# Optimization experiments

Hardware: AMD Instinct MI355X
Metric: run time of the kernel (lower is better)

The kernel has to match this reference:

```python
import jax, jax.numpy as jnp
import numpy as np

N = 50000      # num nodes
E = 800000     # num edges
F_IN = 100     # input features (ogbn-products)
HID = 128      # hidden_dim (per-head out_channels)
H = 2          # heads
OUT = 47       # num classes
NEG_SLOPE = 0.2


def setup_inputs() -> dict:
    key = jax.random.key(0)
    ks = jax.random.split(key, 14)
    def glorot(k, shape, fan):
        return jax.random.normal(k, shape, jnp.float32) * (1.0 / np.sqrt(fan))
    x = jax.random.normal(ks[0], (N, F_IN), jnp.float32)
    edge_index = jax.random.randint(ks[1], (2, E), 0, N)
    # GAT layer 0: lin_l (= lin_r, shared) weight [H*HID, F_IN], attention vecs [H, HID]
    W0 = glorot(ks[2], (H * HID, F_IN), F_IN)
    b0 = jnp.zeros((H * HID,), jnp.float32)
    attl0 = glorot(ks[3], (H, HID), HID)
    attr0 = glorot(ks[4], (H, HID), HID)
    # GAT layer 1: input dim H*HID
    W1 = glorot(ks[5], (H * HID, H * HID), H * HID)
    b1 = jnp.zeros((H * HID,), jnp.float32)
    attl1 = glorot(ks[6], (H, HID), HID)
    attr1 = glorot(ks[7], (H, HID), HID)
    # post_mp: Linear(H*HID -> HID), Linear(HID -> OUT)
    Wp1 = glorot(ks[8], (HID, H * HID), H * HID)
    bp1 = jnp.zeros((HID,), jnp.float32)
    Wp2 = glorot(ks[9], (OUT, HID), HID)
    bp2 = jnp.zeros((OUT,), jnp.float32)
    return dict(x=x, edge_index=edge_index, W0=W0, b0=b0, attl0=attl0, attr0=attr0,
                W1=W1, b1=b1, attl1=attl1, attr1=attr1,
                Wp1=Wp1, bp1=bp1, Wp2=Wp2, bp2=bp2)


def gat_layer(x, W, b, att_l, att_r, src, dst):
    # shared lin_l == lin_r in the source
    h = (x @ W.T + b).reshape(-1, H, HID)          # [N, H, C]
    alpha_l = jnp.einsum('nhc,hc->nh', h, att_l)   # per-node left scores
    alpha_r = jnp.einsum('nhc,hc->nh', h, att_r)   # per-node right scores
    e = jax.nn.leaky_relu(alpha_l[src] + alpha_r[dst], NEG_SLOPE)  # [E, H]
    # segment softmax over edges grouped by destination node
    emax = jax.ops.segment_max(e, dst, num_segments=N)             # [N, H]
    ee = jnp.exp(e - emax[dst])
    denom = jax.ops.segment_sum(ee, dst, num_segments=N)           # [N, H]
    a = ee / denom[dst]                                            # [E, H]
    msg = a[:, :, None] * h[src]                                   # [E, H, C]
    out = jax.ops.segment_sum(msg, dst, num_segments=N)            # [N, H, C]
    return out.reshape(-1, H * HID)


def reference(x, edge_index, W0, b0, attl0, attr0, W1, b1, attl1, attr1, Wp1, bp1, Wp2, bp2):
    src, dst = edge_index[0], edge_index[1]
    x = jax.nn.relu(gat_layer(x, W0, b0, attl0, attr0, src, dst))
    x = jax.nn.relu(gat_layer(x, W1, b1, attl1, attr1, src, dst))
    h = x @ Wp1.T + bp1           # dropout p=0.0 -> identity
    logits = h @ Wp2.T + bp2
    return jax.nn.log_softmax(logits, axis=1)
```

## Files before the change

### kernel.cpp

```cpp
#include <hip/hip_runtime.h>
#include <math.h>

#define N_NODES 50000
#define E_EDGES 800000
#define F_IN 100
#define HID 128
#define HEADS 2
#define OUT_C 47
#define HH (HEADS*HID)
#define MPAD 50176
#define SLOTS 64

typedef float floatx4 __attribute__((ext_vector_type(4)));
typedef float float2v __attribute__((ext_vector_type(2)));
typedef short short8 __attribute__((ext_vector_type(8)));

__device__ inline ushort bf16round(float v) {
    unsigned u = __float_as_uint(v);
    return (ushort)((u + 0x7FFFu + ((u >> 16) & 1u)) >> 16);
}

__device__ __forceinline__ void gl_lds16(const void* g, void* l) {
    __builtin_amdgcn_global_load_lds(
        (const __attribute__((address_space(1))) unsigned int*)g,
        (__attribute__((address_space(3))) unsigned int*)l, 16, 0, 0);
}

__device__ __forceinline__ void gemm_body(
    int bx, int by,
    const ushort* __restrict__ Ab, const ushort* __restrict__ Wb,
    const float* __restrict__ bias,
    ushort* __restrict__ Hb,
    const float* __restrict__ attl, const float* __restrict__ attr,
    float* __restrict__ al, float* __restrict__ ar,
    int M, int Kp, ushort* sA, ushort* sB)
{
    const int t = threadIdx.x;
    const int wave = t >> 6, lane = t & 63;
    const int quad = lane >> 4, l16 = lane & 15;
    const int rl = lane >> 2, seg = lane & 3;
    const int m0 = by * 64, n0 = bx * 128;

    floatx4 acc[8];
#pragma unroll
    for (int j = 0; j < 8; j++) acc[j] = (floatx4)(0.f);

    for (int k0 = 0; k0 < Kp; k0 += 32) {
        {
            size_t gro = (size_t)(m0 + wave * 16 + rl) * Kp + k0 + seg * 8;
            gl_lds16(Ab + gro, sA + (wave * 16) * 32);
        }
#pragma unroll
        for (int j = 0; j < 2; j++) {
            int br = wave * 32 + j * 16;
            size_t gro = (size_t)(n0 + br + rl) * Kp + k0 + seg * 8;
            gl_lds16(Wb + gro, sB + br * 32);
        }
        __syncthreads();

        short8 af = *(const short8*)(sA + (wave * 16 + l16) * 32 + quad * 8);
#pragma unroll
        for (int sn = 0; sn < 8; sn++) {
            int r = sn * 16 + l16;
            short8 b = *(const short8*)(sB + r * 32 + quad * 8);
            acc[sn] = __builtin_amdgcn_mfma_f32_16x16x32_bf16(af, b, acc[sn], 0, 0, 0);
        }
        __syncthreads();
    }

    float bias_r[8], att_l[8], att_r[8];
#pragma unroll
    for (int sn = 0; sn < 8; sn++) {
        int ai = n0 + sn * 16 + l16;
        bias_r[sn] = bias[ai];
        att_l[sn] = attl[ai];
        att_r[sn] = attr[ai];
    }
#pragma unroll
    for (int r = 0; r < 4; r++) {
        int gm = m0 + wave * 16 + quad * 4 + r;
        float suml = 0.f, sumr = 0.f;
#pragma unroll
        for (int sn = 0; sn < 8; sn++) {
            float v = acc[sn][r] + bias_r[sn];
            suml += v * att_l[sn];
            sumr += v * att_r[sn];
            if (gm < M) {
                int gn = n0 + sn * 16 + l16;
                Hb[(size_t)gm * 256 + gn] = bf16round(v);
            }
        }
#pragma unroll
        for (int off = 1; off < 16; off <<= 1) {
            suml += __shfl_xor(suml, off);
            sumr += __shfl_xor(sumr, off);
        }
        if (l16 == 0 && gm < M) {
            al[gm * HEADS + bx] = suml;
            ar[gm * HEADS + bx] = sumr;
        }
    }
}

__global__ __launch_bounds__(256) void gemm_l0(
    const ushort* __restrict__ xb, const ushort* __restrict__ W0b,
    const float* __restrict__ b0,
    const float* __restrict__ attl0, const float* __restrict__ attr0,
    ushort* __restrict__ hb, float* __restrict__ al, float* __restrict__ ar)
{
    __shared__ ushort sA[64 * 32], sB[128 * 32];
    const int g = blockIdx.x;
    const int bx = (g >> 3) & 1;
    const int by = (g >> 4) * 8 + (g & 7);
    gemm_body(bx, by, xb, W0b, b0,
              hb, attl0, attr0, al, ar, N_NODES, 128, sA, sB);
}

__global__ __launch_bounds__(256) void gemm_l1(
    const ushort* __restrict__ Ab, const ushort* __restrict__ Wb,
    const float* __restrict__ bias, ushort* __restrict__ Hb,
    const float* __restrict__ attl, const float* __restrict__ attr,
    float* __restrict__ al, float* __restrict__ ar)
{
    __shared__ ushort sA[64 * 32], sB[128 * 32];
    const int g = blockIdx.x;
    const int bx = (g >> 3) & 1;
    const int by = (g >> 4) * 8 + (g & 7);
    gemm_body(bx, by, Ab, Wb, bias,
              Hb, attl, attr, al, ar, N_NODES, HH, sA, sB);
}

__global__ void count_convert(const int* __restrict__ srcv, const int* __restrict__ dstv,
                              int* __restrict__ deg, ushort* __restrict__ csr16,
                              const float* __restrict__ x,  const float* __restrict__ W0,
                              const float* __restrict__ W1, const float* __restrict__ Wp1,
                              const float* __restrict__ Wp2,
                              ushort* __restrict__ xb,  ushort* __restrict__ W0b,
                              ushort* __restrict__ W1b, ushort* __restrict__ Wp1b,
                              ushort* __restrict__ Wp2b) {
    const int cx = N_NODES * 32;
    const int c0 = cx + 256 * 32;
    const int c1 = c0 + (HH * HH) / 4;
    const int c2 = c1 + (HID * HH) / 4;
    const int c3 = c2 + (64 * HID) / 4;
    int i = blockIdx.x * 256 + threadIdx.x;
    if (i < E_EDGES) {
        int d = dstv[i];
        int r = atomicAdd(&deg[d], 1);
        csr16[(size_t)d * SLOTS + r] = (ushort)srcv[i];
    }
    if (i >= c3) return;
    float4 v = make_float4(0.f, 0.f, 0.f, 0.f);
    ushort* H; size_t o;
    if (i < cx) {
        int row = i >> 5, kc = (i & 31) * 4;
        if (kc < F_IN) v = *(const float4*)(x + (size_t)row * F_IN + kc);
        H = xb; o = (size_t)row * 128 + kc;
    } else if (i < c0) {
        int j = i - cx;
        int row = j >> 5, kc = (j & 31) * 4;
        if (kc < F_IN) v = *(const float4*)(W0 + (size_t)row * F_IN + kc);
        H = W0b; o = (size_t)row * 128 + kc;
    } else if (i < c1) {
        int j = i - c0;
        v = *(const float4*)(W1 + (size_t)j * 4);
        H = W1b; o = (size_t)j * 4;
    } else if (i < c2) {
        int j = i - c1;
        v = *(const float4*)(Wp1 + (size_t)j * 4);
        H = Wp1b; o = (size_t)j * 4;
    } else {
        int j = i - c2;
        int row = j >> 5;
        if (row < OUT_C) v = *(const float4*)(Wp2 + (size_t)j * 4);
        H = Wp2b; o = (size_t)j * 4;
    }
    ushort4 r;
    r.x = bf16round(v.x); r.y = bf16round(v.y);
    r.z = bf16round(v.z); r.w = bf16round(v.w);
    *(ushort4*)(H + o) = r;
}

__global__ __launch_bounds__(256) void gat_aggregate(
    const ushort* __restrict__ hb, const float* __restrict__ al, const float* __restrict__ ar,
    const int* __restrict__ deg, const ushort* __restrict__ csr16,
    ushort* __restrict__ outb)
{
    const int g = blockIdx.x;
    const int xcd = g & 7;
    const int head = xcd & 1;
    const int rank = (g >> 3) * 4 + (xcd >> 1);
    const int wave = threadIdx.x >> 6;
    const int node = rank * 4 + wave;
    const int lane = threadIdx.x & 63;
    const int grp = lane >> 4, c = lane & 15;
    if (node >= N_NODES) return;
    const int n = deg[node];
    const float ard = ar[node * HEADS + head];
    const ushort* __restrict__ hbh = hb + head * HID + c * 8;

    float dsum = 0.f;
    float2v av[4];
#pragma unroll
    for (int j = 0; j < 4; j++) av[j] = (float2v)(0.f);

    int s = 0; float w = 0.f;
    if (lane < n) {
        s = (int)csr16[(size_t)node * SLOTS + lane];
        float e = al[s * HEADS + head] + ard;
        e = fmaxf(e, 0.f) + 0.2f * fminf(e, 0.f);
        w = __expf(e);
        dsum = w;
    }
    for (int i = 0; i < n; i += 8) {
        int e0 = i + grp, e1 = i + 4 + grp;
        int   s0 = __shfl(s, e0);
        float w0 = __shfl(w, e0);
        int   s1 = __shfl(s, e1);
        float w1 = __shfl(w, e1);
        uint4 q0 = make_uint4(0u, 0u, 0u, 0u);
        uint4 q1 = make_uint4(0u, 0u, 0u, 0u);
        if (e0 < n) q0 = *(const uint4*)(hbh + (size_t)s0 * 256);
        if (e1 < n) q1 = *(const uint4*)(hbh + (size_t)s1 * 256);
        float2v we0 = (float2v)(w0);
        float2v we1 = (float2v)(w1);
        float2v p;
        p.x = __uint_as_float(q0.x << 16); p.y = __uint_as_float(q0.x & 0xFFFF0000u);
        av[0] += we0 * p;
        p.x = __uint_as_float(q0.y << 16); p.y = __uint_as_float(q0.y & 0xFFFF0000u);
        av[1] += we0 * p;
        p.x = __uint_as_float(q0.z << 16); p.y = __uint_as_float(q0.z & 0xFFFF0000u);
        av[2] += we0 * p;
        p.x = __uint_as_float(q0.w << 16); p.y = __uint_as_float(q0.w & 0xFFFF0000u);
        av[3] += we0 * p;
        p.x = __uint_as_float(q1.x << 16); p.y = __uint_as_float(q1.x & 0xFFFF0000u);
        av[0] += we1 * p;
        p.x = __uint_as_float(q1.y << 16); p.y = __uint_as_float(q1.y & 0xFFFF0000u);
        av[1] += we1 * p;
        p.x = __uint_as_float(q1.z << 16); p.y = __uint_as_float(q1.z & 0xFFFF0000u);
        av[2] += we1 * p;
        p.x = __uint_as_float(q1.w << 16); p.y = __uint_as_float(q1.w & 0xFFFF0000u);
        av[3] += we1 * p;
    }
#pragma unroll
    for (int j = 0; j < 4; j++) {
        av[j].x += __shfl_xor(av[j].x, 16);
        av[j].y += __shfl_xor(av[j].y, 16);
        av[j].x += __shfl_xor(av[j].x, 32);
        av[j].y += __shfl_xor(av[j].y, 32);
    }
#pragma unroll
    for (int off = 32; off; off >>= 1) dsum += __shfl_xor(dsum, off);

    if (grp == 0) {
        const float inv = (n > 0) ? 1.f / dsum : 0.f;
        ushort r[8];
#pragma unroll
        for (int j = 0; j < 4; j++) {
            r[2*j]   = bf16round(fmaxf(av[j].x * inv, 0.f));
            r[2*j+1] = bf16round(fmaxf(av[j].y * inv, 0.f));
        }
        *(uint4*)(outb + (size_t)node * 256 + head * HID + c * 8) = *(uint4*)r;
    }
}

__global__ __launch_bounds__(256) void fused_post(
    const ushort* __restrict__ Ab,
    const ushort* __restrict__ Bb,
    const float* __restrict__ bp1,
    const ushort* __restrict__ W2b,
    const float* __restrict__ bp2,
    float* __restrict__ out, int M)
{
    __shared__ ushort sA[64 * 32];
    __shared__ ushort sB[128 * 32];
    __shared__ ushort sP[64 * 136];

    const int t = threadIdx.x;
    const int wave = t >> 6, lane = t & 63;
    const int quad = lane >> 4, l16 = lane & 15;
    const int rl = lane >> 2, seg = lane & 3;
    const int m0 = blockIdx.x * 64;

    floatx4 acc[8];
#pragma unroll
    for (int j = 0; j < 8; j++) acc[j] = (floatx4)(0.f);

    for (int k0 = 0; k0 < HH; k0 += 32) {
        {
            size_t gro = (size_t)(m0 + wave * 16 + rl) * HH + k0 + seg * 8;
            gl_lds16(Ab + gro, sA + (wave * 16) * 32);
        }
#pragma unroll
        for (int j = 0; j < 2; j++) {
            int br = wave * 32 + j * 16;
            size_t gro = (size_t)(br + rl) * HH + k0 + seg * 8;
            gl_lds16(Bb + gro, sB + br * 32);
        }
        __syncthreads();
        short8 af = *(const short8*)(sA + (wave * 16 + l16) * 32 + quad * 8);
#pragma unroll
        for (int sn = 0; sn < 8; sn++) {
            short8 b = *(const short8*)(sB + (sn * 16 + l16) * 32 + quad * 8);
            acc[sn] = __builtin_amdgcn_mfma_f32_16x16x32_bf16(af, b, acc[sn], 0, 0, 0);
        }
        __syncthreads();
    }
#pragma unroll
    for (int sn = 0; sn < 8; sn++)
#pragma unroll
        for (int r = 0; r < 4; r++) {
            int row = wave * 16 + quad * 4 + r;
            int col = sn * 16 + l16;
            sP[row * 136 + col] = bf16round(acc[sn][r] + bp1[col]);
        }
    __syncthreads();

    floatx4 acc2[4];
#pragma unroll
    for (int j = 0; j < 4; j++) acc2[j] = (floatx4)(0.f);

    for (int k0 = 0; k0 < HID; k0 += 32) {
        {
            int br = wave * 16;
            size_t gro = (size_t)(br + rl) * HID + k0 + seg * 8;
            gl_lds16(W2b + gro, sA + br * 32);
        }
        __syncthreads();
        short8 ph = *(const short8*)(sP + (wave * 16 + l16) * 136 + k0 + quad * 8);
#pragma unroll
        for (int sn = 0; sn < 4; sn++) {
            short8 b = *(const short8*)(sA + (sn * 16 + l16) * 32 + quad * 8);
            acc2[sn] = __builtin_amdgcn_mfma_f32_16x16x32_bf16(ph, b, acc2[sn], 0, 0, 0);
        }
        __syncthreads();
    }

    float b2[4];
#pragma unroll
    for (int sn = 0; sn < 4; sn++) {
        int n = sn * 16 + l16;
        b2[sn] = (n < OUT_C) ? bp2[n] : 0.f;
    }
#pragma unroll
    for (int r = 0; r < 4; r++) {
        float v[4];
        float m = -INFINITY;
#pragma unroll
        for (int sn = 0; sn < 4; sn++) {
            int n = sn * 16 + l16;
            float xv = (n < OUT_C) ? acc2[sn][r] + b2[sn] : -INFINITY;
            v[sn] = xv;
            m = fmaxf(m, xv);
        }
#pragma unroll
        for (int off = 1; off < 16; off <<= 1) m = fmaxf(m, __shfl_xor(m, off));
        float ssum = 0.f;
#pragma unroll
        for (int sn = 0; sn < 4; sn++) {
            int n = sn * 16 + l16;
            if (n < OUT_C) ssum += __expf(v[sn] - m);
        }
#pragma unroll
        for (int off = 1; off < 16; off <<= 1) ssum += __shfl_xor(ssum, off);
        float lse = m + logf(ssum);
        int gm = m0 + wave * 16 + quad * 4 + r;
        if (gm < M) {
#pragma unroll
            for (int sn = 0; sn < 4; sn++) {
                int n = sn * 16 + l16;
                if (n < OUT_C) out[(size_t)gm * OUT_C + n] = v[sn] - lse;
            }
        }
    }
}

extern "C" void kernel_launch(void* const* d_in, const int* in_sizes, int n_in,
                              void* d_out, int out_size, void* d_ws, size_t ws_size,
                              hipStream_t stream) {
    const float* x     = (const float*)d_in[0];
    const int*   ei    = (const int*)d_in[1];
    const float* W0    = (const float*)d_in[2];
    const float* b0    = (const float*)d_in[3];
    const float* attl0 = (const float*)d_in[4];
    const float* attr0 = (const float*)d_in[5];
    const float* W1    = (const float*)d_in[6];
    const float* b1    = (const float*)d_in[7];
    const float* attl1 = (const float*)d_in[8];
    const float* attr1 = (const float*)d_in[9];
    const float* Wp1   = (const float*)d_in[10];
    const float* bp1   = (const float*)d_in[11];
    const float* Wp2   = (const float*)d_in[12];
    const float* bp2   = (const float*)d_in[13];
    float* out = (float*)d_out;

    const int Nn = N_NODES, Etot = E_EDGES;
    const int* srcv = ei;
    const int* dstv = ei + Etot;

    char* ws = (char*)d_ws;
    size_t off = 0;
    auto alloc = [&](size_t bytes) -> void* {
        void* p = ws + off;
        off = (off + bytes + 255) & ~(size_t)255;
        return p;
    };
    int*    deg    = (int*)alloc((size_t)Nn * sizeof(int));
    ushort* csr16  = (ushort*)alloc((size_t)Nn * SLOTS * 2);
    float*  al     = (float*)alloc((size_t)Nn * HEADS * sizeof(float));
    float*  ar     = (float*)alloc((size_t)Nn * HEADS * sizeof(float));
    ushort* xb     = (ushort*)alloc((size_t)MPAD * 128 * 2);
    ushort* W0b    = (ushort*)alloc((size_t)HH * 128 * 2);
    ushort* W1b    = (ushort*)alloc((size_t)HH * HH * 2);
    ushort* Wp1b   = (ushort*)alloc((size_t)HID * HH * 2);
    ushort* Wp2b   = (ushort*)alloc((size_t)64 * HID * 2);
    ushort* hb     = (ushort*)alloc((size_t)MPAD * HH * 2);
    ushort* xbb    = (ushort*)alloc((size_t)MPAD * HH * 2);

    hipMemsetAsync(deg, 0, (size_t)Nn * sizeof(int), stream);

    {
        const int tot = N_NODES * 32 + 256 * 32 + (HH * HH) / 4 + (HID * HH) / 4 + (64 * HID) / 4;
        const int grid = (tot + 255) / 256;
        count_convert<<<grid, 256, 0, stream>>>(
            srcv, dstv, deg, csr16, x, W0, W1, Wp1, Wp2, xb, W0b, W1b, Wp1b, Wp2b);
    }

    gemm_l0<<<2 * (MPAD / 64), 256, 0, stream>>>(xb, W0b, b0, attl0, attr0, hb, al, ar);

    gat_aggregate<<<25000, 256, 0, stream>>>(hb, al, ar, deg, csr16, xbb);

    gemm_l1<<<2 * (MPAD / 64), 256, 0, stream>>>(xbb, W1b, b1, hb, attl1, attr1, al, ar);

    gat_aggregate<<<25000, 256, 0, stream>>>(hb, al, ar, deg, csr16, xbb);

    fused_post<<<MPAD / 64, 256, 0, stream>>>(xbb, Wp1b, bp1, Wp2b, bp2, out, Nn);
}
```

Before: 288.4 us.

## Overlap CSR edge scatter with layer-0 GEMM and drop degree memset

Moves the atomic edge-bucketing work out of the conversion kernel and into the layer-0 GEMM launch. One of every three blocks runs a GEMM tile and the other two scatter edges, so the latency-bound atomics can overlap with matrix work. The degree array is now zeroed inside the prep kernel instead of by a separate memset. The aggregation loop is padded to a multiple of 8 and issues its feature loads unconditionally, relying on zero weights for the padding lanes, and clamps degree to the slot count. The interleaved launch makes GEMM and scatter blocks share the GPU, and the branchless loads fetch extra rows (node 0) for padding edges.

Measured after the change: 287.5 us. Within noise of the previous version (-0.3%).

```diff
diff --git a/kernel.cpp b/kernel.cpp
--- a/kernel.cpp
+++ b/kernel.cpp
@@ -102,53 +102,20 @@
     }
 }
 
-__global__ __launch_bounds__(256) void gemm_l0(
-    const ushort* __restrict__ xb, const ushort* __restrict__ W0b,
-    const float* __restrict__ b0,
-    const float* __restrict__ attl0, const float* __restrict__ attr0,
-    ushort* __restrict__ hb, float* __restrict__ al, float* __restrict__ ar)
-{
-    __shared__ ushort sA[64 * 32], sB[128 * 32];
-    const int g = blockIdx.x;
-    const int bx = (g >> 3) & 1;
-    const int by = (g >> 4) * 8 + (g & 7);
-    gemm_body(bx, by, xb, W0b, b0,
-              hb, attl0, attr0, al, ar, N_NODES, 128, sA, sB);
-}
-
-__global__ __launch_bounds__(256) void gemm_l1(
-    const ushort* __restrict__ Ab, const ushort* __restrict__ Wb,
-    const float* __restrict__ bias, ushort* __restrict__ Hb,
-    const float* __restrict__ attl, const float* __restrict__ attr,
-    float* __restrict__ al, float* __restrict__ ar)
-{
-    __shared__ ushort sA[64 * 32], sB[128 * 32];
-    const int g = blockIdx.x;
-    const int bx = (g >> 3) & 1;
-    const int by = (g >> 4) * 8 + (g & 7);
-    gemm_body(bx, by, Ab, Wb, bias,
-              Hb, attl, attr, al, ar, N_NODES, HH, sA, sB);
-}
-
-__global__ void count_convert(const int* __restrict__ srcv, const int* __restrict__ dstv,
-                              int* __restrict__ deg, ushort* __restrict__ csr16,
-                              const float* __restrict__ x,  const float* __restrict__ W0,
-                              const float* __restrict__ W1, const float* __restrict__ Wp1,
-                              const float* __restrict__ Wp2,
-                              ushort* __restrict__ xb,  ushort* __restrict__ W0b,
-                              ushort* __restrict__ W1b, ushort* __restrict__ Wp1b,
-                              ushort* __restrict__ Wp2b) {
+__global__ void prep(int* __restrict__ deg,
+                     const float* __restrict__ x,  const float* __restrict__ W0,
+                     const float* __restrict__ W1, const float* __restrict__ Wp1,
+                     const float* __restrict__ Wp2,
+                     ushort* __restrict__ xb,  ushort* __restrict__ W0b,
+                     ushort* __restrict__ W1b, ushort* __restrict__ Wp1b,
+                     ushort* __restrict__ Wp2b) {
     const int cx = N_NODES * 32;
     const int c0 = cx + 256 * 32;
     const int c1 = c0 + (HH * HH) / 4;
     const int c2 = c1 + (HID * HH) / 4;
     const int c3 = c2 + (64 * HID) / 4;
     int i = blockIdx.x * 256 + threadIdx.x;
-    if (i < E_EDGES) {
-        int d = dstv[i];
-        int r = atomicAdd(&deg[d], 1);
-        csr16[(size_t)d * SLOTS + r] = (ushort)srcv[i];
-    }
+    if (i < N_NODES) deg[i] = 0;
     if (i >= c3) return;
     float4 v = make_float4(0.f, 0.f, 0.f, 0.f);
     ushort* H; size_t o;
@@ -181,6 +148,49 @@
     *(ushort4*)(H + o) = r;
 }
 
+#define NG 1568
+#define NEB 3136
+__global__ __launch_bounds__(256) void gemm_l0_edges(
+    const ushort* __restrict__ xb, const ushort* __restrict__ W0b,
+    const float* __restrict__ b0,
+    const float* __restrict__ attl0, const float* __restrict__ attr0,
+    ushort* __restrict__ hb, float* __restrict__ al, float* __restrict__ ar,
+    const int* __restrict__ srcv, const int* __restrict__ dstv,
+    int* __restrict__ deg, ushort* __restrict__ csr16)
+{
+    __shared__ ushort sA[64 * 32], sB[128 * 32];
+    const int g = blockIdx.x;
+    if (g % 3 == 0) {
+        const int gm = g / 3;
+        const int bx = (gm >> 3) & 1;
+        const int by = (gm >> 4) * 8 + (gm & 7);
+        gemm_body(bx, by, xb, W0b, b0,
+                  hb, attl0, attr0, al, ar, N_NODES, 128, sA, sB);
+    } else {
+        const int eidx = g - (g + 2) / 3;
+        int e = eidx * 256 + threadIdx.x;
+        if (e < E_EDGES) {
+            int d = dstv[e];
+            int r = atomicAdd(&deg[d], 1);
+            if (r < SLOTS) csr16[(size_t)d * SLOTS + r] = (ushort)srcv[e];
+        }
+    }
+}
+
+__global__ __launch_bounds__(256) void gemm_l1(
+    const ushort* __restrict__ Ab, const ushort* __restrict__ Wb,
+    const float* __restrict__ bias, ushort* __restrict__ Hb,
+    const float* __restrict__ attl, const float* __restrict__ attr,
+    float* __restrict__ al, float* __restrict__ ar)
+{
+    __shared__ ushort sA[64 * 32], sB[128 * 32];
+    const int g = blockIdx.x;
+    const int bx = (g >> 3) & 1;
+    const int by = (g >> 4) * 8 + (g & 7);
+    gemm_body(bx, by, Ab, Wb, bias,
+              Hb, attl, attr, al, ar, N_NODES, HH, sA, sB);
+}
+
 __global__ __launch_bounds__(256) void gat_aggregate(
     const ushort* __restrict__ hb, const float* __restrict__ al, const float* __restrict__ ar,
     const int* __restrict__ deg, const ushort* __restrict__ csr16,
@@ -194,8 +204,7 @@
     const int node = rank * 4 + wave;
     const int lane = threadIdx.x & 63;
     const int grp = lane >> 4, c = lane & 15;
-    if (node >= N_NODES) return;
-    const int n = deg[node];
+    const int n = min(deg[node], SLOTS);
     const float ard = ar[node * HEADS + head];
     const ushort* __restrict__ hbh = hb + head * HID + c * 8;
 
@@ -212,16 +221,15 @@
         w = __expf(e);
         dsum = w;
     }
-    for (int i = 0; i < n; i += 8) {
+    const int nn = (n + 7) & ~7;
+    for (int i = 0; i < nn; i += 8) {
         int e0 = i + grp, e1 = i + 4 + grp;
         int   s0 = __shfl(s, e0);
         float w0 = __shfl(w, e0);
         int   s1 = __shfl(s, e1);
         float w1 = __shfl(w, e1);
-        uint4 q0 = make_uint4(0u, 0u, 0u, 0u);
-        uint4 q1 = make_uint4(0u, 0u, 0u, 0u);
-        if (e0 < n) q0 = *(const uint4*)(hbh + (size_t)s0 * 256);
-        if (e1 < n) q1 = *(const uint4*)(hbh + (size_t)s1 * 256);
+        uint4 q0 = *(const uint4*)(hbh + (size_t)s0 * 256);
+        uint4 q1 = *(const uint4*)(hbh + (size_t)s1 * 256);
         float2v we0 = (float2v)(w0);
         float2v we1 = (float2v)(w1);
         float2v p;
@@ -417,16 +425,14 @@
     ushort* hb     = (ushort*)alloc((size_t)MPAD * HH * 2);
     ushort* xbb    = (ushort*)alloc((size_t)MPAD * HH * 2);
 
-    hipMemsetAsync(deg, 0, (size_t)Nn * sizeof(int), stream);
-
     {
         const int tot = N_NODES * 32 + 256 * 32 + (HH * HH) / 4 + (HID * HH) / 4 + (64 * HID) / 4;
-        const int grid = (tot + 255) / 256;
-        count_convert<<<grid, 256, 0, stream>>>(
-            srcv, dstv, deg, csr16, x, W0, W1, Wp1, Wp2, xb, W0b, W1b, Wp1b, Wp2b);
-    }
-
-    gemm_l0<<<2 * (MPAD / 64), 256, 0, stream>>>(xb, W0b, b0, attl0, attr0, hb, al, ar);
+        prep<<<(tot + 255) / 256, 256, 0, stream>>>(
+            deg, x, W0, W1, Wp1, Wp2, xb, W0b, W1b, Wp1b, Wp2b);
+    }
+
+    gemm_l0_edges<<<NG + NEB, 256, 0, stream>>>(
+        xb, W0b, b0, attl0, attr0, hb, al, ar, srcv, dstv, deg, csr16);
 
     gat_aggregate<<<25000, 256, 0, stream>>>(hb, al, ar, deg, csr16, xbb);
 
```
